# Kernel optimization log

Hardware: AMD Instinct MI355X
Metric: run time of the kernel (lower is better)

## Reference

```python
import jax, jax.numpy as jnp
import numpy as np

N_NODES = 50000
N_EDGES = 600000
IN_FEATS = 128
HIDDEN = 128
BN_EPS = 1e-5


def setup_inputs() -> dict:
    key = jax.random.key(0)
    ks = jax.random.split(key, 8)
    inputs = jax.random.normal(ks[0], (N_NODES, IN_FEATS), dtype=jnp.float32)
    edge_index = jax.random.randint(ks[1], (2, N_EDGES), 0, N_NODES, dtype=jnp.int64)
    # GraphConv weights (glorot-like scale)
    W1 = jax.random.normal(ks[2], (IN_FEATS, HIDDEN), dtype=jnp.float32) / np.sqrt(IN_FEATS)
    b1 = jnp.zeros((HIDDEN,), jnp.float32)
    W2 = jax.random.normal(ks[3], (HIDDEN, HIDDEN), dtype=jnp.float32) / np.sqrt(HIDDEN)
    b2 = jnp.zeros((HIDDEN,), jnp.float32)
    # BatchNorm1d affine params
    gamma1 = jnp.ones((HIDDEN,), jnp.float32)
    beta1 = jnp.zeros((HIDDEN,), jnp.float32)
    gamma2 = jnp.ones((HIDDEN,), jnp.float32)
    beta2 = jnp.zeros((HIDDEN,), jnp.float32)
    # PReLU (single shared slope, torch default 0.25)
    a1 = jnp.full((1,), 0.25, jnp.float32)
    a2 = jnp.full((1,), 0.25, jnp.float32)
    return {"inputs": inputs, "W1": W1, "b1": b1, "gamma1": gamma1, "beta1": beta1,
            "a1": a1, "W2": W2, "b2": b2, "gamma2": gamma2, "beta2": beta2,
            "a2": a2, "edge_index": edge_index}


def _graph_conv(x, W, b, src, dst, norm_src, norm_dst):
    # DGL GraphConv, norm='both': D_dst^{-1/2} A (D_src^{-1/2} x W) + b
    h = (x * norm_src) @ W                          # [N, H]
    agg = jax.ops.segment_sum(h[src], dst, num_segments=x.shape[0])  # scatter-add
    return agg * norm_dst + b


def _batch_norm(h, gamma, beta):
    mean = jnp.mean(h, axis=0)
    var = jnp.var(h, axis=0)  # biased, as torch BN normalization
    return (h - mean) * jax.lax.rsqrt(var + BN_EPS) * gamma + beta


def _prelu(h, a):
    return jnp.where(h >= 0, h, a * h)


def reference(inputs, W1, b1, gamma1, beta1, a1, W2, b2, gamma2, beta2, a2, edge_index):
    src, dst = edge_index[0], edge_index[1]
    n = inputs.shape[0]
    ones = jnp.ones((src.shape[0],), jnp.float32)
    deg_out = jax.ops.segment_sum(ones, src, num_segments=n)
    deg_in = jax.ops.segment_sum(ones, dst, num_segments=n)
    norm_src = jax.lax.rsqrt(jnp.clip(deg_out, 1.0))[:, None]
    norm_dst = jax.lax.rsqrt(jnp.clip(deg_in, 1.0))[:, None]

    h = _graph_conv(inputs, W1, b1, src, dst, norm_src, norm_dst)
    h = _prelu(_batch_norm(h, gamma1, beta1), a1)
    h = _graph_conv(h, W2, b2, src, dst, norm_src, norm_dst)
    h = _prelu(_batch_norm(h, gamma2, beta2), a2)
    return h
```

## Files before the change

### kernel.cpp

```cpp
#include <hip/hip_runtime.h>

#define HID 128
#define BN_EPS 1e-5f
#define CHUNK 8
#define CAP 64
#define G1_GEMM_BLOCKS 512
#define G1_FILL_BLOCKS 586

typedef __attribute__((ext_vector_type(8))) short bf16x8;
typedef __attribute__((ext_vector_type(4))) float f32x4;

__device__ __forceinline__ float bf2f(unsigned short u) {
  union { unsigned int i; float f; } c; c.i = ((unsigned int)u) << 16; return c.f;
}
__device__ __forceinline__ unsigned short f2bf(float f) {
  union { float f; unsigned int i; } c; c.f = f;
  unsigned int u = c.i;
  return (unsigned short)((u + 0x7FFFu + ((u >> 16) & 1u)) >> 16);
}
__device__ __forceinline__ void unpack8(uint4 u, float* f) {
  f[0] = bf2f((unsigned short)(u.x & 0xffffu)); f[1] = bf2f((unsigned short)(u.x >> 16));
  f[2] = bf2f((unsigned short)(u.y & 0xffffu)); f[3] = bf2f((unsigned short)(u.y >> 16));
  f[4] = bf2f((unsigned short)(u.z & 0xffffu)); f[5] = bf2f((unsigned short)(u.z >> 16));
  f[6] = bf2f((unsigned short)(u.w & 0xffffu)); f[7] = bf2f((unsigned short)(u.w >> 16));
}

__global__ __launch_bounds__(256) void k_norm(const int* __restrict__ cnt,
                                              float* __restrict__ nsnd, int total) {
  int i = blockIdx.x * blockDim.x + threadIdx.x;
  if (i < total) nsnd[i] = rsqrtf(fmaxf((float)cnt[i], 1.0f));
}

__global__ __launch_bounds__(256) void k_prep_w2(const float* __restrict__ W1,
                                                 unsigned short* __restrict__ Wt1,
                                                 const float* __restrict__ W2,
                                                 unsigned short* __restrict__ Wt2) {
  int id = blockIdx.x * 256 + threadIdx.x;
  const float* W = (id < HID * HID) ? W1 : W2;
  unsigned short* Wt = (id < HID * HID) ? Wt1 : Wt2;
  int lid = id & (HID * HID - 1);
  int nn = lid >> 7, kk = lid & 127;
  Wt[lid] = f2bf(W[kk * HID + nn]);
}

template <int MODE>
__device__ __forceinline__ void gemm_body(const void* __restrict__ Xin,
                                          const unsigned short* __restrict__ Wt,
                                          const float* __restrict__ ns,
                                          const float* PS, const float* PH,
                                          float slope,
                                          unsigned short* __restrict__ Gb, int n,
                                          int blk, int nblocks,
                                          unsigned short (*stile)[16 * 136]) {
  const int wib = threadIdx.x >> 6;
  const int lane = threadIdx.x & 63;
  const int c = lane & 15;
  const int g = lane >> 4;
  const int nrb = (n + 15) >> 4;
  const int nw = nblocks * 4;

  bf16x8 bfr[8][4];
#pragma unroll
  for (int ct = 0; ct < 8; ++ct)
#pragma unroll
    for (int kt = 0; kt < 4; ++kt)
      bfr[ct][kt] = *reinterpret_cast<const bf16x8*>(Wt + (ct * 16 + c) * HID + kt * 32 + g * 8);

  for (int w = blk * 4 + wib; w < nrb; w += nw) {
    const int row0 = w * 16;
    int arow = row0 + c;
    if (arow > n - 1) arow = n - 1;
    bf16x8 afr[4];
    if (MODE == 0) {
      const float* X = (const float*)Xin;
#pragma unroll
      for (int kt = 0; kt < 4; ++kt) {
        const float* p = X + (size_t)arow * HID + kt * 32 + g * 8;
        float4 v0 = *reinterpret_cast<const float4*>(p);
        float4 v1 = *reinterpret_cast<const float4*>(p + 4);
        bf16x8 a;
        a[0] = (short)f2bf(v0.x); a[1] = (short)f2bf(v0.y);
        a[2] = (short)f2bf(v0.z); a[3] = (short)f2bf(v0.w);
        a[4] = (short)f2bf(v1.x); a[5] = (short)f2bf(v1.y);
        a[6] = (short)f2bf(v1.z); a[7] = (short)f2bf(v1.w);
        afr[kt] = a;
      }
    } else {
      const unsigned short* Xb = (const unsigned short*)Xin;
      const float sc = ns[arow];
#pragma unroll
      for (int kt = 0; kt < 4; ++kt) {
        const int k0 = kt * 32 + g * 8;
        uint4 u = *reinterpret_cast<const uint4*>(Xb + (size_t)arow * HID + k0);
        float f[8];
        unpack8(u, f);
        float4 s0 = *reinterpret_cast<const float4*>(PS + k0);
        float4 s1 = *reinterpret_cast<const float4*>(PS + k0 + 4);
        float4 h0 = *reinterpret_cast<const float4*>(PH + k0);
        float4 h1 = *reinterpret_cast<const float4*>(PH + k0 + 4);
        float t;
        t = fmaf(f[0], s0.x, h0.x); f[0] = (t >= 0.f ? t : slope * t) * sc;
        t = fmaf(f[1], s0.y, h0.y); f[1] = (t >= 0.f ? t : slope * t) * sc;
        t = fmaf(f[2], s0.z, h0.z); f[2] = (t >= 0.f ? t : slope * t) * sc;
        t = fmaf(f[3], s0.w, h0.w); f[3] = (t >= 0.f ? t : slope * t) * sc;
        t = fmaf(f[4], s1.x, h1.x); f[4] = (t >= 0.f ? t : slope * t) * sc;
        t = fmaf(f[5], s1.y, h1.y); f[5] = (t >= 0.f ? t : slope * t) * sc;
        t = fmaf(f[6], s1.z, h1.z); f[6] = (t >= 0.f ? t : slope * t) * sc;
        t = fmaf(f[7], s1.w, h1.w); f[7] = (t >= 0.f ? t : slope * t) * sc;
        bf16x8 a;
        a[0] = (short)f2bf(f[0]); a[1] = (short)f2bf(f[1]);
        a[2] = (short)f2bf(f[2]); a[3] = (short)f2bf(f[3]);
        a[4] = (short)f2bf(f[4]); a[5] = (short)f2bf(f[5]);
        a[6] = (short)f2bf(f[6]); a[7] = (short)f2bf(f[7]);
        afr[kt] = a;
      }
    }

    f32x4 acc[8];
#pragma unroll
    for (int ct = 0; ct < 8; ++ct) acc[ct] = (f32x4){0.f, 0.f, 0.f, 0.f};
#pragma unroll
    for (int kt = 0; kt < 4; ++kt)
#pragma unroll
      for (int ct = 0; ct < 8; ++ct)
        acc[ct] = __builtin_amdgcn_mfma_f32_16x16x32_bf16(afr[kt], bfr[ct][kt], acc[ct], 0, 0, 0);

#pragma unroll
    for (int ct = 0; ct < 8; ++ct)
#pragma unroll
      for (int q = 0; q < 4; ++q)
        stile[wib][(g * 4 + q) * 136 + ct * 16 + c] = f2bf(acc[ct][q]);

#pragma unroll
    for (int p = 0; p < 4; ++p) {
      int rl = p * 4 + g;
      int grow = row0 + rl;
      if (grow < n) {
        uint4 v = *reinterpret_cast<const uint4*>(&stile[wib][rl * 136 + c * 8]);
        *reinterpret_cast<uint4*>(Gb + (size_t)grow * HID + c * 8) = v;
      }
    }
  }
}

__global__ __launch_bounds__(256) void k_gemm1_fill(const float* __restrict__ X,
                                                    const unsigned short* __restrict__ Wt,
                                                    unsigned short* __restrict__ Gb, int n,
                                                    const int* __restrict__ src,
                                                    const int* __restrict__ dst,
                                                    int* cnt, int* __restrict__ bucket,
                                                    int E, int N) {
  __shared__ __align__(16) unsigned short stile[4][16 * 136];
  if (blockIdx.x >= G1_GEMM_BLOCKS) {
    const int base = ((blockIdx.x - G1_GEMM_BLOCKS) * 256 + threadIdx.x) * 4;
    if (base + 3 < E) {
      int4 s4 = *reinterpret_cast<const int4*>(src + base);
      int4 d4 = *reinterpret_cast<const int4*>(dst + base);
      atomicAdd(&cnt[s4.x], 1);
      atomicAdd(&cnt[s4.y], 1);
      atomicAdd(&cnt[s4.z], 1);
      atomicAdd(&cnt[s4.w], 1);
      int p0 = atomicAdd(&cnt[N + d4.x], 1);
      int p1 = atomicAdd(&cnt[N + d4.y], 1);
      int p2 = atomicAdd(&cnt[N + d4.z], 1);
      int p3 = atomicAdd(&cnt[N + d4.w], 1);
      if (p0 < CAP) bucket[d4.x * CAP + p0] = s4.x;
      if (p1 < CAP) bucket[d4.y * CAP + p1] = s4.y;
      if (p2 < CAP) bucket[d4.z * CAP + p2] = s4.z;
      if (p3 < CAP) bucket[d4.w * CAP + p3] = s4.w;
    } else {
      for (int i = base; i < E; ++i) {
        int s = src[i];
        int d = dst[i];
        atomicAdd(&cnt[s], 1);
        int pos = atomicAdd(&cnt[N + d], 1);
        if (pos < CAP) bucket[d * CAP + pos] = s;
      }
    }
    return;
  }
  gemm_body<0>(X, Wt, nullptr, nullptr, nullptr, 0.f, Gb, n, blockIdx.x,
               G1_GEMM_BLOCKS, stile);
}

__global__ __launch_bounds__(256) void k_gemm2(const unsigned short* __restrict__ Xb,
                                               const unsigned short* __restrict__ Wt,
                                               const float* __restrict__ ns,
                                               const float* __restrict__ ST,
                                               const float* __restrict__ gamma,
                                               const float* __restrict__ beta,
                                               const float* __restrict__ aslope,
                                               unsigned short* __restrict__ Gb, int n,
                                               float invN) {
  __shared__ __align__(16) unsigned short stile[4][16 * 136];
  __shared__ float sPS[HID], sPH[HID];
  if (threadIdx.x < HID) {
    const int t = threadIdx.x;
    float m = ST[t] * invN;
    float var = ST[HID + t] * invN - m * m;
    float sc = gamma[t] * rsqrtf(var + BN_EPS);
    sPS[t] = sc;
    sPH[t] = beta[t] - m * sc;
  }
  __syncthreads();
  gemm_body<1>(Xb, Wt, ns, sPS, sPH, aslope[0], Gb, n, blockIdx.x, gridDim.x, stile);
}

template <int NSMODE>
__global__ __launch_bounds__(256) void k_agg_finish(const unsigned short* __restrict__ H,
                                                    const int* __restrict__ bucket,
                                                    const int* __restrict__ cntD,
                                                    const float* __restrict__ ns,
                                                    const float* __restrict__ nd,
                                                    const float* __restrict__ bias,
                                                    unsigned short* __restrict__ OUT,
                                                    float* stats, int n) {
  const int lane = threadIdx.x & 31;
  const int slot = threadIdx.x >> 5;
  const int rstride = gridDim.x * 16;
  const float4 bj = reinterpret_cast<const float4*>(bias)[lane];
  float4 s = {0.f, 0.f, 0.f, 0.f}, sq = {0.f, 0.f, 0.f, 0.f};

  for (int i0 = blockIdx.x * 16 + slot * 2; i0 < n; i0 += rstride) {
    const int iA = i0, iB = i0 + 1;
    const int lenA = min(cntD[iA], CAP), lenB = min(cntD[iB], CAP);
    const int bA = iA * CAP, bB = iB * CAP;
    const int maxlen = max(lenA, lenB);
    float4 accA = {0.f, 0.f, 0.f, 0.f}, accB = {0.f, 0.f, 0.f, 0.f};
    for (int e = 0; e < maxlen; e += CHUNK) {
      int idxA[CHUNK], idxB[CHUNK];
#pragma unroll
      for (int k = 0; k < CHUNK; ++k) {
        int iAk = bucket[bA + max(min(e + k, lenA - 1), 0)];
        int iBk = bucket[bB + max(min(e + k, lenB - 1), 0)];
        idxA[k] = min(max(iAk, 0), n - 1);
        idxB[k] = min(max(iBk, 0), n - 1);
      }
      uint2 vA[CHUNK], vB[CHUNK];
      float wA[CHUNK], wB[CHUNK];
#pragma unroll
      for (int k = 0; k < CHUNK; ++k) {
        vA[k] = *reinterpret_cast<const uint2*>(H + (size_t)idxA[k] * HID + lane * 4);
        vB[k] = *reinterpret_cast<const uint2*>(H + (size_t)idxB[k] * HID + lane * 4);
        if (NSMODE) { wA[k] = ns[idxA[k]]; wB[k] = ns[idxB[k]]; }
      }
#pragma unroll
      for (int k = 0; k < CHUNK; ++k) {
        if (e + k < lenA) {
          const float wk = NSMODE ? wA[k] : 1.0f;
          accA.x += bf2f((unsigned short)(vA[k].x & 0xffffu)) * wk;
          accA.y += bf2f((unsigned short)(vA[k].x >> 16)) * wk;
          accA.z += bf2f((unsigned short)(vA[k].y & 0xffffu)) * wk;
          accA.w += bf2f((unsigned short)(vA[k].y >> 16)) * wk;
        }
        if (e + k < lenB) {
          const float wk = NSMODE ? wB[k] : 1.0f;
          accB.x += bf2f((unsigned short)(vB[k].x & 0xffffu)) * wk;
          accB.y += bf2f((unsigned short)(vB[k].x >> 16)) * wk;
          accB.z += bf2f((unsigned short)(vB[k].y & 0xffffu)) * wk;
          accB.w += bf2f((unsigned short)(vB[k].y >> 16)) * wk;
        }
      }
    }
    const float ndA = nd[iA], ndB = nd[iB];
    float4 oA, oB;
    oA.x = accA.x * ndA + bj.x; oA.y = accA.y * ndA + bj.y;
    oA.z = accA.z * ndA + bj.z; oA.w = accA.w * ndA + bj.w;
    oB.x = accB.x * ndB + bj.x; oB.y = accB.y * ndB + bj.y;
    oB.z = accB.z * ndB + bj.z; oB.w = accB.w * ndB + bj.w;
    uint2 pkA, pkB;
    pkA.x = (unsigned int)f2bf(oA.x) | ((unsigned int)f2bf(oA.y) << 16);
    pkA.y = (unsigned int)f2bf(oA.z) | ((unsigned int)f2bf(oA.w) << 16);
    pkB.x = (unsigned int)f2bf(oB.x) | ((unsigned int)f2bf(oB.y) << 16);
    pkB.y = (unsigned int)f2bf(oB.z) | ((unsigned int)f2bf(oB.w) << 16);
    *reinterpret_cast<uint2*>(OUT + (size_t)iA * HID + lane * 4) = pkA;
    *reinterpret_cast<uint2*>(OUT + (size_t)iB * HID + lane * 4) = pkB;
    s.x += oA.x + oB.x; s.y += oA.y + oB.y;
    s.z += oA.z + oB.z; s.w += oA.w + oB.w;
    sq.x += oA.x * oA.x + oB.x * oB.x; sq.y += oA.y * oA.y + oB.y * oB.y;
    sq.z += oA.z * oA.z + oB.z * oB.z; sq.w += oA.w * oA.w + oB.w * oB.w;
  }

  __shared__ float red[2][8][HID];
  *reinterpret_cast<float4*>(&red[0][slot][lane * 4]) = s;
  *reinterpret_cast<float4*>(&red[1][slot][lane * 4]) = sq;
  __syncthreads();
  const int t = threadIdx.x;
  if (t < HID) {
    float a = 0.f;
#pragma unroll
    for (int k = 0; k < 8; ++k) a += red[0][k][t];
    atomicAdd(&stats[t], a);
  } else {
    const int j = t - HID;
    float a = 0.f;
#pragma unroll
    for (int k = 0; k < 8; ++k) a += red[1][k][j];
    atomicAdd(&stats[HID + j], a);
  }
}

__global__ __launch_bounds__(256) void k_bn_final(const unsigned short* __restrict__ IN,
                                                  float* __restrict__ OUT,
                                                  const float* __restrict__ ST,
                                                  const float* __restrict__ gamma,
                                                  const float* __restrict__ beta,
                                                  const float* __restrict__ a, int total4,
                                                  float invN) {
  __shared__ float sPS[HID], sPH[HID];
  if (threadIdx.x < HID) {
    const int t = threadIdx.x;
    float m = ST[t] * invN;
    float var = ST[HID + t] * invN - m * m;
    float sc = gamma[t] * rsqrtf(var + BN_EPS);
    sPS[t] = sc;
    sPH[t] = beta[t] - m * sc;
  }
  __syncthreads();
  const float slope = a[0];
  const int stride = gridDim.x * blockDim.x;
  for (int i = blockIdx.x * blockDim.x + threadIdx.x; i < total4; i += stride) {
    int j4 = i & 31;
    float4 ps = reinterpret_cast<const float4*>(sPS)[j4];
    float4 ph = reinterpret_cast<const float4*>(sPH)[j4];
    uint2 u = *reinterpret_cast<const uint2*>(IN + (size_t)i * 4);
    float4 o;
    float t;
    t = fmaf(bf2f((unsigned short)(u.x & 0xffffu)), ps.x, ph.x); o.x = t >= 0.f ? t : slope * t;
    t = fmaf(bf2f((unsigned short)(u.x >> 16)),     ps.y, ph.y); o.y = t >= 0.f ? t : slope * t;
    t = fmaf(bf2f((unsigned short)(u.y & 0xffffu)), ps.z, ph.z); o.z = t >= 0.f ? t : slope * t;
    t = fmaf(bf2f((unsigned short)(u.y >> 16)),     ps.w, ph.w); o.w = t >= 0.f ? t : slope * t;
    reinterpret_cast<float4*>(OUT)[i] = o;
  }
}

extern "C" void kernel_launch(void* const* d_in, const int* in_sizes, int n_in,
                              void* d_out, int out_size, void* d_ws, size_t ws_size,
                              hipStream_t stream) {
  const float* X   = (const float*)d_in[0];
  const float* W1  = (const float*)d_in[1];
  const float* b1  = (const float*)d_in[2];
  const float* g1  = (const float*)d_in[3];
  const float* be1 = (const float*)d_in[4];
  const float* a1  = (const float*)d_in[5];
  const float* W2  = (const float*)d_in[6];
  const float* b2  = (const float*)d_in[7];
  const float* g2  = (const float*)d_in[8];
  const float* be2 = (const float*)d_in[9];
  const float* a2  = (const float*)d_in[10];
  const int*   ei  = (const int*)d_in[11];

  const int N = in_sizes[0] / HID;
  const int E = in_sizes[11] / 2;
  const int* src = ei;
  const int* dst = ei + E;

  float* out = (float*)d_out;

  int* bucket = (int*)d_out;

  unsigned short* bufA = (unsigned short*)d_ws;
  unsigned short* bufB = bufA + (size_t)N * HID;
  int*   cnt     = (int*)(bufB + (size_t)N * HID);
  float* NSND    = (float*)(cnt + 2 * (size_t)N);
  float* ST      = NSND + 2 * (size_t)N;
  unsigned short* Wt1 = (unsigned short*)(ST + 512);
  unsigned short* Wt2 = Wt1 + HID * HID;

  const float invN = 1.0f / (float)N;

  hipMemsetAsync(cnt, 0, 2 * (size_t)N * sizeof(int), stream);
  hipMemsetAsync(ST, 0, 512 * sizeof(float), stream);

  k_prep_w2<<<(2 * HID * HID + 255) / 256, 256, 0, stream>>>(W1, Wt1, W2, Wt2);

  k_gemm1_fill<<<G1_GEMM_BLOCKS + G1_FILL_BLOCKS, 256, 0, stream>>>(
      X, Wt1, bufA, N, src, dst, cnt, bucket, E, N);

  k_norm<<<(2 * N + 255) / 256, 256, 0, stream>>>(cnt, NSND, 2 * N);

  k_agg_finish<1><<<1024, 256, 0, stream>>>(bufA, bucket, cnt + N, NSND, NSND + N, b1,
                                            bufB, ST, N);

  k_gemm2<<<512, 256, 0, stream>>>(bufB, Wt2, NSND, ST, g1, be1, a1, bufA, N, invN);
  k_agg_finish<0><<<1024, 256, 0, stream>>>(bufA, bucket, cnt + N, NSND, NSND + N, b2,
                                            bufB, ST + 256, N);
  k_bn_final<<<2048, 256, 0, stream>>>(bufB, out, ST + 256, g2, be2, a2,
                                       N * (HID / 4), invN);
}
```

Measured before the change: 203.9 us.

## Drop norm kernel, compute degree norms inline, vectorize bucket index loads

Removes the separate k_norm launch and its buffer; degree normalization is now computed on the fly from the counts inside the aggregation and second GEMM kernels. The two memsets are merged into one. The edge fill loop becomes a grid-stride scalar loop over more blocks, and bucket indices are read as int4 vectors instead of clamped scalar loads. This trades a launch and a pass over memory for extra rsqrt work per gathered edge. The vector bucket loads no longer clamp to the valid length, so entries past the count are read, though they are masked out when accumulating.

After: 207.4 us. No clear change (+1.7%).

```diff
diff --git a/kernel.cpp b/kernel.cpp
--- a/kernel.cpp
+++ b/kernel.cpp
@@ -5,7 +5,7 @@
 #define CHUNK 8
 #define CAP 64
 #define G1_GEMM_BLOCKS 512
-#define G1_FILL_BLOCKS 586
+#define G1_FILL_BLOCKS 1024
 
 typedef __attribute__((ext_vector_type(8))) short bf16x8;
 typedef __attribute__((ext_vector_type(4))) float f32x4;
@@ -24,11 +24,8 @@
   f[4] = bf2f((unsigned short)(u.z & 0xffffu)); f[5] = bf2f((unsigned short)(u.z >> 16));
   f[6] = bf2f((unsigned short)(u.w & 0xffffu)); f[7] = bf2f((unsigned short)(u.w >> 16));
 }
-
-__global__ __launch_bounds__(256) void k_norm(const int* __restrict__ cnt,
-                                              float* __restrict__ nsnd, int total) {
-  int i = blockIdx.x * blockDim.x + threadIdx.x;
-  if (i < total) nsnd[i] = rsqrtf(fmaxf((float)cnt[i], 1.0f));
+__device__ __forceinline__ float degnorm(int c) {
+  return rsqrtf(fmaxf((float)c, 1.0f));
 }
 
 __global__ __launch_bounds__(256) void k_prep_w2(const float* __restrict__ W1,
@@ -46,7 +43,7 @@
 template <int MODE>
 __device__ __forceinline__ void gemm_body(const void* __restrict__ Xin,
                                           const unsigned short* __restrict__ Wt,
-                                          const float* __restrict__ ns,
+                                          const int* __restrict__ cntS,
                                           const float* PS, const float* PH,
                                           float slope,
                                           unsigned short* __restrict__ Gb, int n,
@@ -87,7 +84,7 @@
       }
     } else {
       const unsigned short* Xb = (const unsigned short*)Xin;
-      const float sc = ns[arow];
+      const float sc = degnorm(cntS[arow]);
 #pragma unroll
       for (int kt = 0; kt < 4; ++kt) {
         const int k0 = kt * 32 + g * 8;
@@ -152,30 +149,13 @@
                                                     int E, int N) {
   __shared__ __align__(16) unsigned short stile[4][16 * 136];
   if (blockIdx.x >= G1_GEMM_BLOCKS) {
-    const int base = ((blockIdx.x - G1_GEMM_BLOCKS) * 256 + threadIdx.x) * 4;
-    if (base + 3 < E) {
-      int4 s4 = *reinterpret_cast<const int4*>(src + base);
-      int4 d4 = *reinterpret_cast<const int4*>(dst + base);
-      atomicAdd(&cnt[s4.x], 1);
-      atomicAdd(&cnt[s4.y], 1);
-      atomicAdd(&cnt[s4.z], 1);
-      atomicAdd(&cnt[s4.w], 1);
-      int p0 = atomicAdd(&cnt[N + d4.x], 1);
-      int p1 = atomicAdd(&cnt[N + d4.y], 1);
-      int p2 = atomicAdd(&cnt[N + d4.z], 1);
-      int p3 = atomicAdd(&cnt[N + d4.w], 1);
-      if (p0 < CAP) bucket[d4.x * CAP + p0] = s4.x;
-      if (p1 < CAP) bucket[d4.y * CAP + p1] = s4.y;
-      if (p2 < CAP) bucket[d4.z * CAP + p2] = s4.z;
-      if (p3 < CAP) bucket[d4.w * CAP + p3] = s4.w;
-    } else {
-      for (int i = base; i < E; ++i) {
-        int s = src[i];
-        int d = dst[i];
-        atomicAdd(&cnt[s], 1);
-        int pos = atomicAdd(&cnt[N + d], 1);
-        if (pos < CAP) bucket[d * CAP + pos] = s;
-      }
+    const int stride = G1_FILL_BLOCKS * 256;
+    for (int i = (blockIdx.x - G1_GEMM_BLOCKS) * 256 + threadIdx.x; i < E; i += stride) {
+      int s = src[i];
+      int d = dst[i];
+      atomicAdd(&cnt[s], 1);
+      int pos = atomicAdd(&cnt[N + d], 1);
+      if (pos < CAP) bucket[d * CAP + pos] = s;
     }
     return;
   }
@@ -185,7 +165,7 @@
 
 __global__ __launch_bounds__(256) void k_gemm2(const unsigned short* __restrict__ Xb,
                                                const unsigned short* __restrict__ Wt,
-                                               const float* __restrict__ ns,
+                                               const int* __restrict__ cntS,
                                                const float* __restrict__ ST,
                                                const float* __restrict__ gamma,
                                                const float* __restrict__ beta,
@@ -203,38 +183,41 @@
     sPH[t] = beta[t] - m * sc;
   }
   __syncthreads();
-  gemm_body<1>(Xb, Wt, ns, sPS, sPH, aslope[0], Gb, n, blockIdx.x, gridDim.x, stile);
+  gemm_body<1>(Xb, Wt, cntS, sPS, sPH, aslope[0], Gb, n, blockIdx.x, gridDim.x, stile);
 }
 
 template <int NSMODE>
 __global__ __launch_bounds__(256) void k_agg_finish(const unsigned short* __restrict__ H,
                                                     const int* __restrict__ bucket,
-                                                    const int* __restrict__ cntD,
-                                                    const float* __restrict__ ns,
-                                                    const float* __restrict__ nd,
+                                                    const int* __restrict__ cnt,
                                                     const float* __restrict__ bias,
                                                     unsigned short* __restrict__ OUT,
                                                     float* stats, int n) {
   const int lane = threadIdx.x & 31;
   const int slot = threadIdx.x >> 5;
   const int rstride = gridDim.x * 16;
+  const int* cntD = cnt + n;
   const float4 bj = reinterpret_cast<const float4*>(bias)[lane];
   float4 s = {0.f, 0.f, 0.f, 0.f}, sq = {0.f, 0.f, 0.f, 0.f};
 
   for (int i0 = blockIdx.x * 16 + slot * 2; i0 < n; i0 += rstride) {
     const int iA = i0, iB = i0 + 1;
-    const int lenA = min(cntD[iA], CAP), lenB = min(cntD[iB], CAP);
+    const int cA = cntD[iA], cB = cntD[iB];
+    const int lenA = min(cA, CAP), lenB = min(cB, CAP);
     const int bA = iA * CAP, bB = iB * CAP;
     const int maxlen = max(lenA, lenB);
     float4 accA = {0.f, 0.f, 0.f, 0.f}, accB = {0.f, 0.f, 0.f, 0.f};
     for (int e = 0; e < maxlen; e += CHUNK) {
-      int idxA[CHUNK], idxB[CHUNK];
+      int4 rA0 = *reinterpret_cast<const int4*>(bucket + bA + e);
+      int4 rA1 = *reinterpret_cast<const int4*>(bucket + bA + e + 4);
+      int4 rB0 = *reinterpret_cast<const int4*>(bucket + bB + e);
+      int4 rB1 = *reinterpret_cast<const int4*>(bucket + bB + e + 4);
+      int idxA[CHUNK] = {rA0.x, rA0.y, rA0.z, rA0.w, rA1.x, rA1.y, rA1.z, rA1.w};
+      int idxB[CHUNK] = {rB0.x, rB0.y, rB0.z, rB0.w, rB1.x, rB1.y, rB1.z, rB1.w};
 #pragma unroll
       for (int k = 0; k < CHUNK; ++k) {
-        int iAk = bucket[bA + max(min(e + k, lenA - 1), 0)];
-        int iBk = bucket[bB + max(min(e + k, lenB - 1), 0)];
-        idxA[k] = min(max(iAk, 0), n - 1);
-        idxB[k] = min(max(iBk, 0), n - 1);
+        idxA[k] = min(max(idxA[k], 0), n - 1);
+        idxB[k] = min(max(idxB[k], 0), n - 1);
       }
       uint2 vA[CHUNK], vB[CHUNK];
       float wA[CHUNK], wB[CHUNK];
@@ -242,7 +225,10 @@
       for (int k = 0; k < CHUNK; ++k) {
         vA[k] = *reinterpret_cast<const uint2*>(H + (size_t)idxA[k] * HID + lane * 4);
         vB[k] = *reinterpret_cast<const uint2*>(H + (size_t)idxB[k] * HID + lane * 4);
-        if (NSMODE) { wA[k] = ns[idxA[k]]; wB[k] = ns[idxB[k]]; }
+        if (NSMODE) {
+          wA[k] = degnorm(cnt[idxA[k]]);
+          wB[k] = degnorm(cnt[idxB[k]]);
+        }
       }
 #pragma unroll
       for (int k = 0; k < CHUNK; ++k) {
@@ -262,7 +248,7 @@
         }
       }
     }
-    const float ndA = nd[iA], ndB = nd[iB];
+    const float ndA = degnorm(cA), ndB = degnorm(cB);
     float4 oA, oB;
     oA.x = accA.x * ndA + bj.x; oA.y = accA.y * ndA + bj.y;
     oA.z = accA.z * ndA + bj.z; oA.w = accA.w * ndA + bj.w;
@@ -362,29 +348,23 @@
   unsigned short* bufA = (unsigned short*)d_ws;
   unsigned short* bufB = bufA + (size_t)N * HID;
   int*   cnt     = (int*)(bufB + (size_t)N * HID);
-  float* NSND    = (float*)(cnt + 2 * (size_t)N);
-  float* ST      = NSND + 2 * (size_t)N;
+  float* ST      = (float*)(cnt + 2 * (size_t)N);
   unsigned short* Wt1 = (unsigned short*)(ST + 512);
   unsigned short* Wt2 = Wt1 + HID * HID;
 
   const float invN = 1.0f / (float)N;
 
-  hipMemsetAsync(cnt, 0, 2 * (size_t)N * sizeof(int), stream);
-  hipMemsetAsync(ST, 0, 512 * sizeof(float), stream);
+  hipMemsetAsync(cnt, 0, (2 * (size_t)N + 512) * sizeof(int), stream);
 
   k_prep_w2<<<(2 * HID * HID + 255) / 256, 256, 0, stream>>>(W1, Wt1, W2, Wt2);
 
   k_gemm1_fill<<<G1_GEMM_BLOCKS + G1_FILL_BLOCKS, 256, 0, stream>>>(
       X, Wt1, bufA, N, src, dst, cnt, bucket, E, N);
 
-  k_norm<<<(2 * N + 255) / 256, 256, 0, stream>>>(cnt, NSND, 2 * N);
-
-  k_agg_finish<1><<<1024, 256, 0, stream>>>(bufA, bucket, cnt + N, NSND, NSND + N, b1,
-                                            bufB, ST, N);
-
-  k_gemm2<<<512, 256, 0, stream>>>(bufB, Wt2, NSND, ST, g1, be1, a1, bufA, N, invN);
-  k_agg_finish<0><<<1024, 256, 0, stream>>>(bufA, bucket, cnt + N, NSND, NSND + N, b2,
-                                            bufB, ST + 256, N);
+  k_agg_finish<1><<<1024, 256, 0, stream>>>(bufA, bucket, cnt, b1, bufB, ST, N);
+
+  k_gemm2<<<512, 256, 0, stream>>>(bufB, Wt2, cnt, ST, g1, be1, a1, bufA, N, invN);
+  k_agg_finish<0><<<1024, 256, 0, stream>>>(bufA, bucket, cnt, b2, bufB, ST + 256, N);
   k_bn_final<<<2048, 256, 0, stream>>>(bufB, out, ST + 256, g2, be2, a2,
                                        N * (HID / 4), invN);
 }
```
